# Kernel tuning notes

Hardware: AMD Instinct MI355X
Metric: run time of the kernel (lower is better)

Reference implementation:

```python
import jax, jax.numpy as jnp
import numpy as np

B, S, D = 4, 2048, 1024

def setup_inputs() -> dict:
    key = jax.random.key(0)
    kx, kk, kq, kv = jax.random.split(key, 4)
    scale = 1.0 / np.sqrt(D)
    x = jax.random.normal(kx, (B, S, D), dtype=jnp.float32)
    # nn.Linear weights, applied as x @ W.T; init with small scale like torch default
    Wk = jax.random.normal(kk, (D, D), dtype=jnp.float32) * scale
    Wq = jax.random.normal(kq, (D, D), dtype=jnp.float32) * scale
    Wv = jax.random.normal(kv, (D, D), dtype=jnp.float32) * scale
    return {"x": x, "Wk": Wk, "Wq": Wq, "Wv": Wv}

def reference(x, Wk, Wq, Wv):
    # k/q/v: (B, S, D) @ (D, D_out) -- Linear applies W as x @ W.T
    k = jnp.einsum('bsd,kd->bsk', x, Wk)
    q = jnp.einsum('bsd,kd->bsk', x, Wq)
    v = jnp.einsum('bsd,vd->bsv', x, Wv)
    # scaled dot-product scores: (B, S, S)
    scores = jnp.einsum('bqk,bsk->bqs', q, k) / jnp.sqrt(jnp.asarray(k.shape[-1], x.dtype))
    # causal mask: allow j <= i (upper-right masked out)
    S_len = x.shape[1]
    causal = jnp.tril(jnp.ones((S_len, S_len), dtype=bool))
    scores = jnp.where(causal[None, :, :], scores, jnp.asarray(-jnp.inf, x.dtype))
    weights = jax.nn.softmax(scores, axis=-1)
    # dropout is identity in eval / p used as deterministic baseline
    out = jnp.einsum('bqs,bsv->bqv', weights, v)
    return out
```

## Files before the change

kernel.cpp:

```cpp
#include <hip/hip_runtime.h>

typedef __attribute__((ext_vector_type(8))) short bf16x8;
typedef __attribute__((ext_vector_type(4))) float f32x4;
typedef __attribute__((ext_vector_type(4))) unsigned short u16x4;
typedef __attribute__((ext_vector_type(8))) unsigned short u16x8;

#define MFMA16(a, b, c) __builtin_amdgcn_mfma_f32_16x16x32_bf16((a), (b), (c), 0, 0, 0)

__device__ __forceinline__ ushort f2bf(float f) {
    unsigned u = __float_as_uint(f);
    unsigned r = (u + 0x7FFFu + ((u >> 16) & 1u)) >> 16;
    return (ushort)r;
}
__device__ __forceinline__ float bf2f(ushort s) {
    return __uint_as_float(((unsigned)s) << 16);
}

__device__ __forceinline__ void async16(const ushort* g, ushort* l) {
    __builtin_amdgcn_global_load_lds(
        (const __attribute__((address_space(1))) unsigned*)g,
        (__attribute__((address_space(3))) unsigned*)l, 16, 0, 0);
}

#define SBAR()  __builtin_amdgcn_s_barrier()
#define SCHED() __builtin_amdgcn_sched_barrier(0)

__global__ __launch_bounds__(256) void cvt_all(
    const float* __restrict__ x,  const float* __restrict__ wk,
    const float* __restrict__ wq, const float* __restrict__ wv,
    ushort* __restrict__ xb,  ushort* __restrict__ wvb,
    ushort* __restrict__ wkt, ushort* __restrict__ wqt)
{
    __shared__ float t[32][33];
    int bx = blockIdx.x;
    if (bx < 4608) {
        const size_t XN = (size_t)8192 * 1024;
        size_t idx = ((size_t)bx * 256 + threadIdx.x) * 8;
        const float* s;
        ushort* d;
        if (idx < XN) { s = x + idx; d = xb + idx; }
        else          { s = wv + (idx - XN); d = wvb + (idx - XN); }
        float4 a = *(const float4*)s;
        float4 b = *(const float4*)(s + 4);
        u16x8 p;
        p[0] = f2bf(a.x); p[1] = f2bf(a.y); p[2] = f2bf(a.z); p[3] = f2bf(a.w);
        p[4] = f2bf(b.x); p[5] = f2bf(b.y); p[6] = f2bf(b.z); p[7] = f2bf(b.w);
        *(u16x8*)d = p;
    } else {
        bx -= 4608;
        const int z  = bx >> 10;
        const int tb = bx & 1023;
        const int e0 = (tb & 31) * 32, d0 = (tb >> 5) * 32;
        const float* src = z ? wq : wk;
        ushort*      dst = z ? wqt : wkt;
        const int tx = threadIdx.x & 31, ty = threadIdx.x >> 5;
#pragma unroll
        for (int r = 0; r < 4; ++r)
            t[ty + 8 * r][tx] = src[(size_t)(e0 + ty + 8 * r) * 1024 + d0 + tx];
        __syncthreads();
#pragma unroll
        for (int r = 0; r < 4; ++r)
            dst[(size_t)(d0 + ty + 8 * r) * 1024 + e0 + tx] = f2bf(t[tx][ty + 8 * r]);
    }
}

__device__ __forceinline__ void mma_tile(
    const ushort* __restrict__ A, int lda, int abase,
    const ushort* __restrict__ B, int ldb, int bbase,
    int ktiles,
    ushort* As, ushort* Bs, f32x4 (&acc)[4][4])
{
    const int tid  = threadIdx.x;
    const int lane = tid & 63, wid = tid >> 6;
    const int wr = wid >> 1, wc = wid & 1;
    const int lrow = lane & 15, kgrp = lane >> 4;
    const int ci = lane >> 3;
    const int cc = (lane & 7) * 8;

#pragma unroll
    for (int m = 0; m < 4; ++m)
#pragma unroll
        for (int n = 0; n < 4; ++n) acc[m][n] = (f32x4){0.f, 0.f, 0.f, 0.f};

    for (int kt = 0; kt < ktiles; ++kt) {
        const int k0 = kt * 64;
#pragma unroll
        for (int i = 0; i < 4; ++i) {
            const int r = (wid * 4 + i) * 8 + ci;
            async16(&A[(size_t)(abase + r) * lda + k0 + cc], &As[(wid * 4 + i) * 512]);
            async16(&B[(size_t)(bbase + r) * ldb + k0 + cc], &Bs[(wid * 4 + i) * 512]);
        }
        __syncthreads();
#pragma unroll
        for (int kk = 0; kk < 2; ++kk) {
            bf16x8 af[4], bfr[4];
#pragma unroll
            for (int m = 0; m < 4; ++m)
                af[m] = *(const bf16x8*)&As[(wr * 64 + m * 16 + lrow) * 64 + kk * 32 + kgrp * 8];
#pragma unroll
            for (int n = 0; n < 4; ++n)
                bfr[n] = *(const bf16x8*)&Bs[(wc * 64 + n * 16 + lrow) * 64 + kk * 32 + kgrp * 8];
#pragma unroll
            for (int m = 0; m < 4; ++m)
#pragma unroll
                for (int n = 0; n < 4; ++n)
                    acc[m][n] = MFMA16(af[m], bfr[n], acc[m][n]);
        }
        __syncthreads();
    }
}

__device__ __forceinline__ void mma256(
    const ushort* __restrict__ A, int lda, int abase,
    const ushort* __restrict__ B, int ldb, int bbase,
    int NT, ushort* As, ushort* Bs, f32x4 (&acc)[8][4])
{
    const int tid  = threadIdx.x;
    const int lane = tid & 63, w = tid >> 6;
    const int wr = w >> 2, wc = w & 3;
    const int lrow = lane & 15, kgrp = lane >> 4;
    const int srr = lane >> 2;
    const int scc = (lane & 3) * 8;

    auto stage = [&](int t, int isB, int kk) {
        const ushort* src = isB ? B : A;
        const int ld = isB ? ldb : lda;
        const int rb = isB ? bbase : abase;
        ushort* slot = (isB ? Bs : As) + (size_t)(((t & 1) * 2 + kk)) * 8192;
#pragma unroll
        for (int i = 0; i < 2; ++i) {
            const int r = (w * 2 + i) * 16 + srr;
            async16(&src[(size_t)(rb + r) * ld + t * 64 + kk * 32 + scc],
                    slot + (w * 2 + i) * 512);
        }
    };

#pragma unroll
    for (int m = 0; m < 8; ++m)
#pragma unroll
        for (int n = 0; n < 4; ++n) acc[m][n] = (f32x4){0.f, 0.f, 0.f, 0.f};

    stage(0, 0, 0); stage(0, 1, 0); stage(0, 0, 1); stage(0, 1, 1);
    if (NT > 1) {
        stage(1, 0, 0); stage(1, 1, 0);
        asm volatile("s_waitcnt vmcnt(4)" ::: "memory");
    } else {
        asm volatile("s_waitcnt vmcnt(0)" ::: "memory");
    }
    SCHED();
    SBAR();
    SCHED();

    for (int t = 0; t < NT; ++t) {
        ushort* Ab = As + (size_t)(t & 1) * 2 * 8192;
        ushort* Bb = Bs + (size_t)(t & 1) * 2 * 8192;
        bf16x8 af[8], bfr[2];

#pragma unroll
        for (int m = 0; m < 8; ++m)
            af[m] = *(const bf16x8*)&Ab[(wr * 128 + m * 16 + lrow) * 32 + kgrp * 8];
#pragma unroll
        for (int n = 0; n < 2; ++n)
            bfr[n] = *(const bf16x8*)&Bb[(wc * 64 + n * 16 + lrow) * 32 + kgrp * 8];
        if (t + 1 < NT) stage(t + 1, 0, 1);
        SBAR(); SCHED();
        __builtin_amdgcn_s_setprio(1);
#pragma unroll
        for (int m = 0; m < 8; ++m) {
            acc[m][0] = MFMA16(af[m], bfr[0], acc[m][0]);
            acc[m][1] = MFMA16(af[m], bfr[1], acc[m][1]);
        }
        __builtin_amdgcn_s_setprio(0);
        SBAR(); SCHED();

#pragma unroll
        for (int n = 0; n < 2; ++n)
            bfr[n] = *(const bf16x8*)&Bb[(wc * 64 + (2 + n) * 16 + lrow) * 32 + kgrp * 8];
        if (t + 1 < NT) stage(t + 1, 1, 1);
        SBAR(); SCHED();
        __builtin_amdgcn_s_setprio(1);
#pragma unroll
        for (int m = 0; m < 8; ++m) {
            acc[m][2] = MFMA16(af[m], bfr[0], acc[m][2]);
            acc[m][3] = MFMA16(af[m], bfr[1], acc[m][3]);
        }
        __builtin_amdgcn_s_setprio(0);
        SBAR(); SCHED();

#pragma unroll
        for (int m = 0; m < 8; ++m)
            af[m] = *(const bf16x8*)&Ab[8192 + (wr * 128 + m * 16 + lrow) * 32 + kgrp * 8];
#pragma unroll
        for (int n = 0; n < 2; ++n)
            bfr[n] = *(const bf16x8*)&Bb[8192 + (wc * 64 + n * 16 + lrow) * 32 + kgrp * 8];
        if (t + 2 < NT) stage(t + 2, 0, 0);
        SBAR(); SCHED();
        __builtin_amdgcn_s_setprio(1);
#pragma unroll
        for (int m = 0; m < 8; ++m) {
            acc[m][0] = MFMA16(af[m], bfr[0], acc[m][0]);
            acc[m][1] = MFMA16(af[m], bfr[1], acc[m][1]);
        }
        __builtin_amdgcn_s_setprio(0);
        SBAR(); SCHED();

#pragma unroll
        for (int n = 0; n < 2; ++n)
            bfr[n] = *(const bf16x8*)&Bb[8192 + (wc * 64 + (2 + n) * 16 + lrow) * 32 + kgrp * 8];
        if (t + 2 < NT) {
            stage(t + 2, 1, 0);
            asm volatile("s_waitcnt vmcnt(4)" ::: "memory");
        } else if (t + 1 < NT) {
            asm volatile("s_waitcnt vmcnt(0)" ::: "memory");
        }
        SCHED();
        SBAR(); SCHED();
        __builtin_amdgcn_s_setprio(1);
#pragma unroll
        for (int m = 0; m < 8; ++m) {
            acc[m][2] = MFMA16(af[m], bfr[0], acc[m][2]);
            acc[m][3] = MFMA16(af[m], bfr[1], acc[m][3]);
        }
        __builtin_amdgcn_s_setprio(0);
        SBAR(); SCHED();
    }
}

__global__ __launch_bounds__(256) void m_gemm(
    const ushort* __restrict__ Wkt, const ushort* __restrict__ Wqt,
    ushort* __restrict__ Mtr)
{
    __shared__ ushort As[128 * 64];
    __shared__ ushort Bs[128 * 64];
    const int fbase = blockIdx.x * 128;
    const int dbase = blockIdx.y * 128;

    f32x4 acc[4][4];
    mma_tile(Wkt, 1024, fbase, Wqt, 1024, dbase, 16, As, Bs, acc);

    const int lane = threadIdx.x & 63, wid = threadIdx.x >> 6;
    const int wr = wid >> 1, wc = wid & 1;
    const int lrow = lane & 15, kgrp = lane >> 4;
#pragma unroll
    for (int m = 0; m < 4; ++m)
#pragma unroll
        for (int n = 0; n < 4; ++n)
#pragma unroll
            for (int r = 0; r < 4; ++r) {
                const int gf = fbase + wr * 64 + m * 16 + kgrp * 4 + r;
                const int gd = dbase + wc * 64 + n * 16 + lrow;
                Mtr[(size_t)gf * 1024 + gd] = f2bf(acc[m][n][r] * 0.03125f);
            }
}

__global__ __launch_bounds__(512, 2) void tv_gemm8(
    const ushort* __restrict__ xb, const ushort* __restrict__ Mtr,
    const ushort* __restrict__ Wvb,
    ushort* __restrict__ Tb, ushort* __restrict__ Vt)
{
    __shared__ ushort As[2 * 2 * 8192];
    __shared__ ushort Bs[2 * 2 * 8192];

    const int z = blockIdx.z;
    const ushort* Bmat = z ? Wvb : Mtr;
    const int mbase = blockIdx.x * 256;
    const int nbase = blockIdx.y * 256;

    f32x4 acc[8][4];
    mma256(xb, 1024, mbase, Bmat, 1024, nbase, 16, As, Bs, acc);

    const int lane = threadIdx.x & 63, w = threadIdx.x >> 6;
    const int wr = w >> 2, wc = w & 3;
    const int lrow = lane & 15, kgrp = lane >> 4;

    if (z == 1) {
        const int b  = mbase >> 11;
        const int s0 = mbase & 2047;
        ushort* VtB = Vt + (size_t)b * 1024 * 2048;
#pragma unroll
        for (int m = 0; m < 8; ++m)
#pragma unroll
            for (int n = 0; n < 4; ++n) {
                u16x4 pk;
#pragma unroll
                for (int r = 0; r < 4; ++r) pk[r] = f2bf(acc[m][n][r]);
                const int d = nbase + wc * 64 + n * 16 + lrow;
                const int s = s0 + wr * 128 + m * 16 + kgrp * 4;
                *(u16x4*)&VtB[(size_t)d * 2048 + s] = pk;
            }
    } else {
#pragma unroll
        for (int m = 0; m < 8; ++m)
#pragma unroll
            for (int n = 0; n < 4; ++n)
#pragma unroll
                for (int r = 0; r < 4; ++r) {
                    const int gr = mbase + wr * 128 + m * 16 + kgrp * 4 + r;
                    const int gc = nbase + wc * 64 + n * 16 + lrow;
                    Tb[(size_t)gr * 1024 + gc] = f2bf(acc[m][n][r]);
                }
    }
}

__global__ __launch_bounds__(512, 2) void scores_gemm8(
    const ushort* __restrict__ Tb, const ushort* __restrict__ xb,
    ushort* __restrict__ Sall)
{
    __shared__ ushort As[2 * 2 * 8192];
    __shared__ ushort Bs[2 * 2 * 8192];

    ushort* S = Sall + (size_t)blockIdx.y * 2048 * 2048;
    const int rb = blockIdx.y * 2048;

    int t = blockIdx.x;
    int it = (int)((sqrtf(8.0f * (float)t + 1.0f) - 1.0f) * 0.5f);
    while ((it + 1) * (it + 2) / 2 <= t) ++it;
    while (it * (it + 1) / 2 > t) --it;
    const int jt = t - it * (it + 1) / 2;
    const int ibase = it * 256, jbase = jt * 256;
    const bool diag = (it == jt);

    f32x4 acc[8][4];
    mma256(Tb, 1024, rb + ibase, xb, 1024, rb + jbase, 16, As, Bs, acc);

    const int lane = threadIdx.x & 63, w = threadIdx.x >> 6;
    const int wr = w >> 2, wc = w & 3;
    const int lrow = lane & 15, kgrp = lane >> 4;
#pragma unroll
    for (int m = 0; m < 8; ++m)
#pragma unroll
        for (int n = 0; n < 4; ++n)
#pragma unroll
            for (int r = 0; r < 4; ++r) {
                const int gi = ibase + wr * 128 + m * 16 + kgrp * 4 + r;
                const int gj = jbase + wc * 64 + n * 16 + lrow;
                float p = __expf(acc[m][n][r]);
                if (diag && gj > gi) p = 0.f;
                S[(size_t)gi * 2048 + gj] = f2bf(p);
            }
}

__device__ __forceinline__ void pv_sub(
    const ushort* __restrict__ P, const ushort* __restrict__ Vt,
    float* __restrict__ O, int it, int nbase,
    ushort* As, ushort* Bs, float* rs)
{
    const int tid  = threadIdx.x;
    const int lane = tid & 63, w = tid >> 6;
    const int wr = w >> 2, wc = w & 3;
    const int lrow = lane & 15, kgrp = lane >> 4;
    const int srow = lane >> 3;
    const int sc16 = (lane & 7) ^ srow;
    const int pbase = it * 128;
    const int NT = 2 * (it + 1);

    auto stage = [&](int t) {
        ushort* dA = As + (size_t)(t & 1) * 8192;
        ushort* dB = Bs + (size_t)(t & 1) * 8192;
#pragma unroll
        for (int i = 0; i < 2; ++i) {
            const int rr = (i * 8 + w) * 8 + srow;
            async16(&P [(size_t)(pbase + rr) * 2048 + t * 64 + sc16 * 8],
                    dA + ((i * 8 + w) * 64 + lane) * 8);
            async16(&Vt[(size_t)(nbase + rr) * 2048 + t * 64 + sc16 * 8],
                    dB + ((i * 8 + w) * 64 + lane) * 8);
        }
    };

    f32x4 acc[4][2];
#pragma unroll
    for (int m = 0; m < 4; ++m)
#pragma unroll
        for (int n = 0; n < 2; ++n) acc[m][n] = (f32x4){0.f, 0.f, 0.f, 0.f};
    float fs = 0.f;

    stage(0);
    if (NT > 1) { stage(1); asm volatile("s_waitcnt vmcnt(4)" ::: "memory"); }
    else        {           asm volatile("s_waitcnt vmcnt(0)" ::: "memory"); }
    SCHED();
    SBAR(); SCHED();

    for (int t = 0; t < NT; ++t) {
        const ushort* Ab = As + (size_t)(t & 1) * 8192;
        const ushort* Bb = Bs + (size_t)(t & 1) * 8192;
        bf16x8 af[2][4], bq[2][2];
#pragma unroll
        for (int kk = 0; kk < 2; ++kk) {
            const int p16 = (kk * 4 + kgrp) ^ (lrow & 7);
#pragma unroll
            for (int m = 0; m < 4; ++m) {
                const int row = wr * 64 + m * 16 + lrow;
                af[kk][m] = *(const bf16x8*)&Ab[row * 64 + p16 * 8];
            }
#pragma unroll
            for (int n = 0; n < 2; ++n) {
                const int row = wc * 32 + n * 16 + lrow;
                bq[kk][n] = *(const bf16x8*)&Bb[row * 64 + p16 * 8];
            }
        }
        asm volatile("s_waitcnt lgkmcnt(0)" ::: "memory");
        SCHED();
#pragma unroll
        for (int kk = 0; kk < 2; ++kk)
#pragma unroll
            for (int m = 0; m < 4; ++m)
                if (m == wc) {
#pragma unroll
                    for (int e = 0; e < 8; ++e)
                        fs += bf2f((ushort)af[kk][m][e]);
                }
        SBAR(); SCHED();
        if (t + 2 < NT) {
            stage(t + 2);
            asm volatile("s_waitcnt vmcnt(4)" ::: "memory");
        } else if (t + 1 < NT) {
            asm volatile("s_waitcnt vmcnt(0)" ::: "memory");
        }
        SCHED();
        SBAR(); SCHED();
        __builtin_amdgcn_s_setprio(1);
#pragma unroll
        for (int kk = 0; kk < 2; ++kk)
#pragma unroll
            for (int m = 0; m < 4; ++m) {
                acc[m][0] = MFMA16(af[kk][m], bq[kk][0], acc[m][0]);
                acc[m][1] = MFMA16(af[kk][m], bq[kk][1], acc[m][1]);
            }
        __builtin_amdgcn_s_setprio(0);
    }

    fs += __shfl_xor(fs, 16);
    fs += __shfl_xor(fs, 32);
    if (lane < 16) rs[wr * 64 + wc * 16 + lane] = fs;
    __syncthreads();

#pragma unroll
    for (int m = 0; m < 4; ++m)
#pragma unroll
        for (int r = 0; r < 4; ++r) {
            const int ri = wr * 64 + m * 16 + kgrp * 4 + r;
            const float inv = 1.0f / rs[ri];
            const int gi = pbase + ri;
#pragma unroll
            for (int n = 0; n < 2; ++n) {
                const int gc = nbase + wc * 32 + n * 16 + lrow;
                O[(size_t)gi * 1024 + gc] = acc[m][n][r] * inv;
            }
        }
    __syncthreads();
}

__global__ __launch_bounds__(512, 2) void pv_pair(
    const ushort* __restrict__ Pall, const ushort* __restrict__ Vtall,
    float* __restrict__ Oall)
{
    __shared__ ushort As[2 * 8192];
    __shared__ ushort Bs[2 * 8192];
    __shared__ float rs[128];

    const ushort* P  = Pall  + (size_t)blockIdx.z * 2048 * 2048;
    const ushort* Vt = Vtall + (size_t)blockIdx.z * 1024 * 2048;
    float*        O  = Oall  + (size_t)blockIdx.z * 2048 * 1024;
    const int nbase = blockIdx.y * 128;

    pv_sub(P, Vt, O, 15 - (int)blockIdx.x, nbase, As, Bs, rs);
    pv_sub(P, Vt, O, (int)blockIdx.x,      nbase, As, Bs, rs);
}

extern "C" void kernel_launch(void* const* d_in, const int* in_sizes, int n_in,
                              void* d_out, int out_size, void* d_ws, size_t ws_size,
                              hipStream_t stream)
{
    (void)in_sizes; (void)n_in; (void)out_size; (void)ws_size;
    const float* x  = (const float*)d_in[0];
    const float* Wk = (const float*)d_in[1];
    const float* Wq = (const float*)d_in[2];
    const float* Wv = (const float*)d_in[3];
    float* out = (float*)d_out;

    const size_t M1 = (size_t)1024 * 1024;
    ushort* ws  = (ushort*)d_ws;
    ushort* xb  = ws;
    ushort* Tb  = xb  + 8 * M1;
    ushort* Vt  = Tb  + 8 * M1;
    ushort* Sb  = Vt  + 8 * M1;
    ushort* Wkt = Sb  + 16 * M1;
    ushort* Wqt = Wkt + M1;
    ushort* Wvb = Wqt + M1;
    ushort* Mtr = Wvb + M1;

    cvt_all<<<6656, 256, 0, stream>>>(x, Wk, Wq, Wv, xb, Wvb, Wkt, Wqt);
    m_gemm<<<dim3(8, 8), 256, 0, stream>>>(Wkt, Wqt, Mtr);
    tv_gemm8<<<dim3(32, 4, 2), 512, 0, stream>>>(xb, Mtr, Wvb, Tb, Vt);
    scores_gemm8<<<dim3(36, 4), 512, 0, stream>>>(Tb, xb, Sb);
    pv_pair<<<dim3(8, 8, 4), 512, 0, stream>>>(Sb, Vt, out);
}
```

Before: 156.8 us.

## Store full 64-wide K tiles in LDS with XOR swizzle and regroup staging

The shared-memory tile layout in the 256x256 GEMM core changes from two 32-column K halves to a single 64-column row per tile, with an XOR swizzle on the 16-byte groups. Global loads now fetch 128-byte row segments per 8 lanes instead of 64-byte segments, and fragment reads apply the matching swizzle to avoid LDS bank conflicts. The prefetch schedule is reordered so staging is split by row half (hi) rather than by K half, moving both A halves of tile t+2 to the last phase. This is meant to cut bank conflicts and improve global coalescing, but it changes when the B half and A halves land relative to the vmcnt waits, which could expose more latency.

```diff
diff --git a/kernel.cpp b/kernel.cpp
--- a/kernel.cpp
+++ b/kernel.cpp
@@ -119,19 +119,19 @@
     const int lane = tid & 63, w = tid >> 6;
     const int wr = w >> 2, wc = w & 3;
     const int lrow = lane & 15, kgrp = lane >> 4;
-    const int srr = lane >> 2;
-    const int scc = (lane & 3) * 8;
-
-    auto stage = [&](int t, int isB, int kk) {
+    const int sgl  = ((lane & 7) ^ ((lane >> 3) & 7)) * 8;
+    const int srow = lane >> 3;
+
+    auto stage = [&](int t, int isB, int hi) {
         const ushort* src = isB ? B : A;
         const int ld = isB ? ldb : lda;
         const int rb = isB ? bbase : abase;
-        ushort* slot = (isB ? Bs : As) + (size_t)(((t & 1) * 2 + kk)) * 8192;
+        ushort* buf = (isB ? Bs : As) + (size_t)(t & 1) * 16384;
 #pragma unroll
         for (int i = 0; i < 2; ++i) {
-            const int r = (w * 2 + i) * 16 + srr;
-            async16(&src[(size_t)(rb + r) * ld + t * 64 + kk * 32 + scc],
-                    slot + (w * 2 + i) * 512);
+            const int r = hi * 128 + (w * 2 + i) * 8 + srow;
+            async16(&src[(size_t)(rb + r) * ld + t * 64 + sgl],
+                    buf + (size_t)(hi * 128 + (w * 2 + i) * 8) * 64 + lane * 8);
         }
     };
 
@@ -140,9 +140,9 @@
 #pragma unroll
         for (int n = 0; n < 4; ++n) acc[m][n] = (f32x4){0.f, 0.f, 0.f, 0.f};
 
-    stage(0, 0, 0); stage(0, 1, 0); stage(0, 0, 1); stage(0, 1, 1);
+    stage(0, 0, 0); stage(0, 0, 1); stage(0, 1, 0); stage(0, 1, 1);
     if (NT > 1) {
-        stage(1, 0, 0); stage(1, 1, 0);
+        stage(1, 0, 0); stage(1, 0, 1);
         asm volatile("s_waitcnt vmcnt(4)" ::: "memory");
     } else {
         asm volatile("s_waitcnt vmcnt(0)" ::: "memory");
@@ -151,18 +151,23 @@
     SBAR();
     SCHED();
 
+    const int sw = lrow & 7;
+
     for (int t = 0; t < NT; ++t) {
-        ushort* Ab = As + (size_t)(t & 1) * 2 * 8192;
-        ushort* Bb = Bs + (size_t)(t & 1) * 2 * 8192;
+        ushort* Ab = As + (size_t)(t & 1) * 16384;
+        ushort* Bb = Bs + (size_t)(t & 1) * 16384;
         bf16x8 af[8], bfr[2];
 
-#pragma unroll
-        for (int m = 0; m < 8; ++m)
-            af[m] = *(const bf16x8*)&Ab[(wr * 128 + m * 16 + lrow) * 32 + kgrp * 8];
-#pragma unroll
-        for (int n = 0; n < 2; ++n)
-            bfr[n] = *(const bf16x8*)&Bb[(wc * 64 + n * 16 + lrow) * 32 + kgrp * 8];
-        if (t + 1 < NT) stage(t + 1, 0, 1);
+        {
+            const int g = (kgrp ^ sw) * 8;
+#pragma unroll
+            for (int m = 0; m < 8; ++m)
+                af[m] = *(const bf16x8*)&Ab[(wr * 128 + m * 16 + lrow) * 64 + g];
+#pragma unroll
+            for (int n = 0; n < 2; ++n)
+                bfr[n] = *(const bf16x8*)&Bb[(wc * 64 + n * 16 + lrow) * 64 + g];
+        }
+        if (t + 1 < NT) stage(t + 1, 1, 0);
         SBAR(); SCHED();
         __builtin_amdgcn_s_setprio(1);
 #pragma unroll
@@ -173,9 +178,12 @@
         __builtin_amdgcn_s_setprio(0);
         SBAR(); SCHED();
 
-#pragma unroll
-        for (int n = 0; n < 2; ++n)
-            bfr[n] = *(const bf16x8*)&Bb[(wc * 64 + (2 + n) * 16 + lrow) * 32 + kgrp * 8];
+        {
+            const int g = (kgrp ^ sw) * 8;
+#pragma unroll
+            for (int n = 0; n < 2; ++n)
+                bfr[n] = *(const bf16x8*)&Bb[(wc * 64 + (2 + n) * 16 + lrow) * 64 + g];
+        }
         if (t + 1 < NT) stage(t + 1, 1, 1);
         SBAR(); SCHED();
         __builtin_amdgcn_s_setprio(1);
@@ -187,13 +195,15 @@
         __builtin_amdgcn_s_setprio(0);
         SBAR(); SCHED();
 
-#pragma unroll
-        for (int m = 0; m < 8; ++m)
-            af[m] = *(const bf16x8*)&Ab[8192 + (wr * 128 + m * 16 + lrow) * 32 + kgrp * 8];
-#pragma unroll
-        for (int n = 0; n < 2; ++n)
-            bfr[n] = *(const bf16x8*)&Bb[8192 + (wc * 64 + n * 16 + lrow) * 32 + kgrp * 8];
-        if (t + 2 < NT) stage(t + 2, 0, 0);
+        {
+            const int g = ((4 + kgrp) ^ sw) * 8;
+#pragma unroll
+            for (int m = 0; m < 8; ++m)
+                af[m] = *(const bf16x8*)&Ab[(wr * 128 + m * 16 + lrow) * 64 + g];
+#pragma unroll
+            for (int n = 0; n < 2; ++n)
+                bfr[n] = *(const bf16x8*)&Bb[(wc * 64 + n * 16 + lrow) * 64 + g];
+        }
         SBAR(); SCHED();
         __builtin_amdgcn_s_setprio(1);
 #pragma unroll
@@ -204,11 +214,14 @@
         __builtin_amdgcn_s_setprio(0);
         SBAR(); SCHED();
 
-#pragma unroll
-        for (int n = 0; n < 2; ++n)
-            bfr[n] = *(const bf16x8*)&Bb[8192 + (wc * 64 + (2 + n) * 16 + lrow) * 32 + kgrp * 8];
+        {
+            const int g = ((4 + kgrp) ^ sw) * 8;
+#pragma unroll
+            for (int n = 0; n < 2; ++n)
+                bfr[n] = *(const bf16x8*)&Bb[(wc * 64 + (2 + n) * 16 + lrow) * 64 + g];
+        }
         if (t + 2 < NT) {
-            stage(t + 2, 1, 0);
+            stage(t + 2, 0, 0); stage(t + 2, 0, 1);
             asm volatile("s_waitcnt vmcnt(4)" ::: "memory");
         } else if (t + 1 < NT) {
             asm volatile("s_waitcnt vmcnt(0)" ::: "memory");
@@ -258,8 +271,8 @@
     const ushort* __restrict__ Wvb,
     ushort* __restrict__ Tb, ushort* __restrict__ Vt)
 {
-    __shared__ ushort As[2 * 2 * 8192];
-    __shared__ ushort Bs[2 * 2 * 8192];
+    __shared__ ushort As[2 * 16384];
+    __shared__ ushort Bs[2 * 16384];
 
     const int z = blockIdx.z;
     const ushort* Bmat = z ? Wvb : Mtr;
@@ -306,8 +319,8 @@
     const ushort* __restrict__ Tb, const ushort* __restrict__ xb,
     ushort* __restrict__ Sall)
 {
-    __shared__ ushort As[2 * 2 * 8192];
-    __shared__ ushort Bs[2 * 2 * 8192];
+    __shared__ ushort As[2 * 16384];
+    __shared__ ushort Bs[2 * 16384];
 
     ushort* S = Sall + (size_t)blockIdx.y * 2048 * 2048;
     const int rb = blockIdx.y * 2048;
```

Result: faster. 150.5 us (-4.0%).
